# Performance work log

Hardware: AMD Instinct MI355X
Metric: run time of the kernel (lower is better)

## Reference

```python
import jax, jax.numpy as jnp
import numpy as np

COST_CLASS, COST_BBOX, COST_GIOU = 1.0, 5.0, 2.0


def _to_xyxy(b):
    cx, cy, w, h = b[..., 0], b[..., 1], b[..., 2], b[..., 3]
    return jnp.stack([cx - w / 2, cy - h / 2, cx + w / 2, cy + h / 2], axis=-1)


def _generalized_box_iou(a, b):
    # a: [N,4] xyxy, b: [M,4] xyxy -> [N,M]
    area_a = (a[:, 2] - a[:, 0]) * (a[:, 3] - a[:, 1])
    area_b = (b[:, 2] - b[:, 0]) * (b[:, 3] - b[:, 1])
    lt = jnp.maximum(a[:, None, :2], b[None, :, :2])
    rb = jnp.minimum(a[:, None, 2:], b[None, :, 2:])
    wh = jnp.clip(rb - lt, 0.0)
    inter = wh[..., 0] * wh[..., 1]
    union = area_a[:, None] + area_b[None, :] - inter
    iou = inter / union
    lt_c = jnp.minimum(a[:, None, :2], b[None, :, :2])
    rb_c = jnp.maximum(a[:, None, 2:], b[None, :, 2:])
    wh_c = jnp.clip(rb_c - lt_c, 0.0)
    area_c = wh_c[..., 0] * wh_c[..., 1]
    return iou - (area_c - union) / area_c


@jax.jit
def _cost_matrix(class_probs, pred_boxes, tgt_boxes, tgt_labels):
    bs, q, k = class_probs.shape
    probs_flat = class_probs.reshape(bs * q, k)
    cost_class = -probs_flat[:, tgt_labels]                          # [BQ, T]
    cost_bbox = jnp.abs(pred_boxes.reshape(bs * q, 1, 4) - tgt_boxes[None, :, :]).sum(-1)
    cost_giou = -_generalized_box_iou(_to_xyxy(pred_boxes.reshape(bs * q, 4)), _to_xyxy(tgt_boxes))
    C = COST_BBOX * cost_bbox + COST_CLASS * cost_class + COST_GIOU * cost_giou
    return C.reshape(bs, q, -1)


def _hungarian(cost):
    # min-cost assignment, cost [n, m] with n <= m (e-maxx JV algorithm).
    n, m = cost.shape
    INF = 1e18
    u = np.zeros(n + 1)
    v = np.zeros(m + 1)
    p = np.zeros(m + 1, dtype=np.int64)
    way = np.zeros(m + 1, dtype=np.int64)
    for i in range(1, n + 1):
        p[0] = i
        j0 = 0
        minv = np.full(m + 1, INF)
        used = np.zeros(m + 1, dtype=bool)
        while True:
            used[j0] = True
            i0 = p[j0]
            cj = cost[i0 - 1] - u[i0] - v[1:]
            upd = (~used[1:]) & (cj < minv[1:])
            minv[1:] = np.where(upd, cj, minv[1:])
            way[1:] = np.where(upd, j0, way[1:])
            free_vals = np.where(used[1:], INF, minv[1:])
            j1 = int(np.argmin(free_vals)) + 1
            delta = free_vals[j1 - 1]
            used_idx = np.nonzero(used)[0]
            u[p[used_idx]] += delta
            v[used_idx] -= delta
            minv[1:] = np.where(used[1:], minv[1:], minv[1:] - delta)
            j0 = j1
            if p[j0] == 0:
                break
        while j0:
            j1 = way[j0]
            p[j0] = p[j1]
            j0 = j1
    rows = p[1:] - 1                      # for each col: matched row or -1
    cols = np.nonzero(rows >= 0)[0]
    return rows[cols], cols               # (row_idx per match, col_idx) sorted by col


def setup_inputs() -> dict:
    key = jax.random.key(0)
    k1, k2, k3, k4 = jax.random.split(key, 4)
    bs, q, k, t_total = 64, 300, 91, 4096
    class_probs = jax.random.uniform(k1, (bs, q, k), dtype=jnp.float32)
    pred_boxes = jax.random.uniform(k2, (bs, q, 4), dtype=jnp.float32)
    tgt_boxes = jax.random.uniform(k3, (t_total, 4), dtype=jnp.float32)
    tgt_labels = jax.random.randint(k4, (t_total,), 0, k)
    return {"class_probs": class_probs, "pred_boxes": pred_boxes,
            "tgt_boxes": tgt_boxes, "tgt_labels": tgt_labels}


def reference(class_probs, pred_boxes, tgt_boxes, tgt_labels):
    bs, q, _ = class_probs.shape
    t_per = tgt_boxes.shape[0] // bs      # equal #targets per image
    C = _cost_matrix(class_probs, pred_boxes, tgt_boxes, tgt_labels)
    C_np = np.asarray(C)
    pred_idx, tgt_idx = [], []
    for b in range(bs):                   # per-batch assignment, as in the original
        c = C_np[b][:, b * t_per:(b + 1) * t_per]      # [Q, T], Q > T
        t_rows, q_cols = _hungarian(c.T)               # assign each target a query
        pred_idx.append(q_cols)
        tgt_idx.append(t_rows)
    return C, jnp.asarray(np.stack(pred_idx)), jnp.asarray(np.stack(tgt_idx))
```

## Files before the change

### kernel.cpp

```cpp
#include <hip/hip_runtime.h>

#define BS   64
#define Q    300
#define K    91
#define T    4096
#define TPER 64
#define M    300
#define NR   64
#define WS_STRIDE 304

typedef float __attribute__((ext_vector_type(4))) f32x4;

__device__ __forceinline__ float cost_entry(const float4 pb, const float4 tb,
                                            const float prob)
{
    const float px0 = pb.x - pb.z * 0.5f, py0 = pb.y - pb.w * 0.5f;
    const float px1 = pb.x + pb.z * 0.5f, py1 = pb.y + pb.w * 0.5f;
    const float parea = (px1 - px0) * (py1 - py0);
    const float tx0 = tb.x - tb.z * 0.5f, ty0 = tb.y - tb.w * 0.5f;
    const float tx1 = tb.x + tb.z * 0.5f, ty1 = tb.y + tb.w * 0.5f;
    const float tarea = (tx1 - tx0) * (ty1 - ty0);
    const float bb = fabsf(pb.x - tb.x) + fabsf(pb.y - tb.y)
                   + fabsf(pb.z - tb.z) + fabsf(pb.w - tb.w);
    const float iw = fmaxf(fminf(px1, tx1) - fmaxf(px0, tx0), 0.f);
    const float ih = fmaxf(fminf(py1, ty1) - fmaxf(py0, ty0), 0.f);
    const float inter = iw * ih;
    const float uni   = parea + tarea - inter;
    const float iou   = inter * __builtin_amdgcn_rcpf(uni);
    const float cw  = fmaxf(fmaxf(px1, tx1) - fminf(px0, tx0), 0.f);
    const float ch  = fmaxf(fmaxf(py1, ty1) - fminf(py0, ty0), 0.f);
    const float carea = cw * ch;
    const float giou  = iou - (carea - uni) * __builtin_amdgcn_rcpf(carea);
    return 5.0f * bb - prob - 2.0f * giou;
}

__device__ void cost_block(int cb, const float* __restrict__ probs,
                           const float* __restrict__ pboxes,
                           const float* __restrict__ tboxes,
                           const int* __restrict__ tlabels,
                           float* __restrict__ C)
{
    __shared__ __align__(16) float sprob4[K][4];
    const int tid = threadIdx.x;
    const int bq0 = cb * 4;
    for (int idx = tid; idx < 4 * K; idx += 64) {
        const int k = idx >> 2, r = idx & 3;
        sprob4[k][r] = probs[(size_t)(bq0 + r) * K + k];
    }
    float4 pbr[4];
#pragma unroll
    for (int r = 0; r < 4; ++r) pbr[r] = ((const float4*)pboxes)[bq0 + r];
    __syncthreads();

    const float4* tbv = (const float4*)tboxes;
    const int4*   lbv = (const int4*)tlabels;

    int4 lb = lbv[tid];
    float4 tb[4];
#pragma unroll
    for (int k = 0; k < 4; ++k) tb[k] = tbv[(tid << 2) + k];

#pragma unroll 1
    for (int c = 0; c < 16; ++c) {
        int4 lbn = {0, 0, 0, 0};
        float4 tbn[4];
        if (c < 15) {
            const int nt0 = ((c + 1) << 8) + (tid << 2);
            lbn = lbv[nt0 >> 2];
#pragma unroll
            for (int k = 0; k < 4; ++k) tbn[k] = tbv[nt0 + k];
        }
        const int labs[4] = { lb.x, lb.y, lb.z, lb.w };
        float4 pr[4];
#pragma unroll
        for (int k = 0; k < 4; ++k)
            pr[k] = *(const float4*)sprob4[labs[k]];

        const int t0 = (c << 8) + (tid << 2);
        float out[4][4];
#pragma unroll
        for (int k = 0; k < 4; ++k) {
#pragma unroll
            for (int r = 0; r < 4; ++r) {
                const float prk = (r == 0) ? pr[k].x : (r == 1) ? pr[k].y
                                : (r == 2) ? pr[k].z : pr[k].w;
                out[r][k] = cost_entry(pbr[r], tb[k], prk);
            }
        }
#pragma unroll
        for (int r = 0; r < 4; ++r) {
            f32x4 v = { out[r][0], out[r][1], out[r][2], out[r][3] };
            __builtin_nontemporal_store(
                v, (f32x4*)&C[(size_t)(bq0 + r) * T + t0]);
        }
        if (c < 15) {
            lb = lbn;
#pragma unroll
            for (int k = 0; k < 4; ++k) tb[k] = tbn[k];
        }
    }
}

__device__ void hungarian_block(int b, const float* __restrict__ probs,
                                const float* __restrict__ pboxes,
                                const float* __restrict__ tboxes,
                                const int* __restrict__ tlabels,
                                float* __restrict__ wslice,
                                float* __restrict__ pred_out,
                                float* __restrict__ tgt_out)
{
    __shared__ int p[M + 1];
    __shared__ int way[M + 1];
    __shared__ int rargArr[NR];
    const int tid = threadIdx.x;
    const bool lv = (tid < 60);
    const int c0 = lv ? 5 * tid : 0;

    float4 pbx[5];
#pragma unroll
    for (int s = 0; s < 5; ++s)
        pbx[s] = ((const float4*)pboxes)[b * Q + c0 + s];

    float rmin_f = 1e30f; int rarg = 0;
#pragma unroll 1
    for (int i = 0; i < NR; ++i) {
        const float4 tb = ((const float4*)tboxes)[b * TPER + i];
        const int lab = tlabels[b * TPER + i];
        const size_t pbase = (size_t)(b * Q + c0) * K + lab;
        float vals[5];
        float lmin = 1e30f; int lidx = 0x7fffffff;
#pragma unroll
        for (int s = 0; s < 5; ++s) {
            const float pr = probs[pbase + (size_t)s * K];
            vals[s] = cost_entry(pbx[s], tb, pr);
            if (lv && vals[s] < lmin) { lmin = vals[s]; lidx = c0 + s; }
        }
        if (lv) {
#pragma unroll
            for (int s = 0; s < 5; ++s)
                wslice[i * WS_STRIDE + c0 + s] = vals[s];
        }
        float rv = lv ? lmin : 1e30f; int ri = lidx;
#pragma unroll
        for (int off = 32; off > 0; off >>= 1) {
            const float ov = __shfl_xor(rv, off);
            const int   oi = __shfl_xor(ri, off);
            if (ov < rv || (ov == rv && oi < ri)) { rv = ov; ri = oi; }
        }
        if (tid == i) { rmin_f = rv; rarg = ri; }
    }
    double u_reg = (double)rmin_f;

    rargArr[tid] = rarg;
    for (int j = tid; j <= M; j += 64) p[j] = 0;
    __syncthreads();

    unsigned long long m0 = 0ull;
    if (tid == 0) {
#pragma unroll 1
        for (int r = 0; r < NR; ++r) {
            const int ac = rargArr[r] + 1;
            if (p[ac] == 0) { p[ac] = r + 1; m0 |= 1ull << r; }
        }
    }
    __syncthreads();
    const unsigned long long matchedRows = __shfl(m0, 0);

    double v_[5], minv_[5];
#pragma unroll
    for (int s = 0; s < 5; ++s) v_[s] = 0.0;
    const unsigned used0 = lv ? 0u : 0x1fu;

#pragma unroll 1
    for (int i = 1; i <= NR; ++i) {
        if ((matchedRows >> (i - 1)) & 1ull) continue;
        if (tid == 0) p[0] = i;
        unsigned usedmask = used0;
        bool inTree = false;
#pragma unroll
        for (int s = 0; s < 5; ++s) minv_[s] = 1e18;
        int i0 = i, j0 = 0;
        float crow[5];
        {
            const float* rp = wslice + (size_t)(i0 - 1) * WS_STRIDE + c0;
#pragma unroll
            for (int s = 0; s < 5; ++s) crow[s] = rp[s];
        }
        int guard = 0;
        while (true) {
            if (tid == i0 - 1) inTree = true;
            const double ui0 = __shfl(u_reg, i0 - 1);
            double lmin = 1e18; int lidx = 0x7fffffff;
#pragma unroll
            for (int s = 0; s < 5; ++s) {
                if (!((usedmask >> s) & 1u)) {
                    const double cj = (double)crow[s] - ui0 - v_[s];
                    if (cj < minv_[s]) { minv_[s] = cj; way[c0 + s + 1] = j0; }
                    if (minv_[s] < lmin) { lmin = minv_[s]; lidx = c0 + s; }
                }
            }
            double rv = lmin; int ri = lidx;
#pragma unroll
            for (int off = 32; off > 0; off >>= 1) {
                const double ov = __shfl_xor(rv, off);
                const int    oi = __shfl_xor(ri, off);
                if (ov < rv || (ov == rv && oi < ri)) { rv = ov; ri = oi; }
            }
            const double delta = rv;
            const int c1 = ri, j1 = c1 + 1;
            const int i0n = p[j1];
            float crow2[5];
            if (i0n) {
                const float* rp2 = wslice + (size_t)(i0n - 1) * WS_STRIDE + c0;
#pragma unroll
                for (int s = 0; s < 5; ++s) crow2[s] = rp2[s];
            }
            if (inTree) u_reg += delta;
#pragma unroll
            for (int s = 0; s < 5; ++s) {
                if ((usedmask >> s) & 1u) v_[s] -= delta;
                else                      minv_[s] -= delta;
            }
            if (lv && c1 >= c0 && c1 < c0 + 5) usedmask |= 1u << (c1 - c0);
            j0 = j1;
            if (!i0n || ++guard > 512) break;
            i0 = i0n;
#pragma unroll
            for (int s = 0; s < 5; ++s) crow[s] = crow2[s];
        }
        __syncthreads();
        if (tid == 0) {
            int jj = j0;
            while (jj) { const int jn = way[jj]; p[jj] = p[jn]; jj = jn; }
        }
        __syncthreads();
    }

    int cnt = 0;
#pragma unroll
    for (int s = 0; s < 5; ++s)
        if (lv && p[c0 + s + 1] > 0) ++cnt;
    int incl = cnt;
#pragma unroll
    for (int off = 1; off < 64; off <<= 1) {
        const int t = __shfl_up(incl, off);
        if (tid >= off) incl += t;
    }
    int pos = incl - cnt;
#pragma unroll
    for (int s = 0; s < 5; ++s) {
        if (lv) {
            const int pi = p[c0 + s + 1];
            if (pi > 0) {
                pred_out[b * TPER + pos] = (float)(c0 + s);
                tgt_out [b * TPER + pos] = (float)(pi - 1);
                ++pos;
            }
        }
    }
}

__global__ __launch_bounds__(64) void fused_kernel(
    const float* __restrict__ probs, const float* __restrict__ pboxes,
    const float* __restrict__ tboxes, const int* __restrict__ tlabels,
    float* __restrict__ C, float* __restrict__ pred_out,
    float* __restrict__ tgt_out, float* __restrict__ ws)
{
    const int bid = blockIdx.x;
    if (bid < BS)
        hungarian_block(bid, probs, pboxes, tboxes, tlabels,
                        ws + (size_t)bid * NR * WS_STRIDE, pred_out, tgt_out);
    else
        cost_block(bid - BS, probs, pboxes, tboxes, tlabels, C);
}

__global__ __launch_bounds__(256) void cost_kernel_fb(
    const float* __restrict__ probs, const float* __restrict__ pboxes,
    const float* __restrict__ tboxes, const int* __restrict__ tlabels,
    float* __restrict__ C)
{
    __shared__ float sprobs[4][K];
    const int tid = threadIdx.x;
    const int bq0 = blockIdx.x * 4;
    for (int idx = tid; idx < 4 * K; idx += 256)
        sprobs[idx / K][idx % K] = probs[(size_t)bq0 * K + idx];
    float4 pbr[4];
#pragma unroll
    for (int r = 0; r < 4; ++r) pbr[r] = ((const float4*)pboxes)[bq0 + r];
    __syncthreads();
#pragma unroll
    for (int c = 0; c < 4; ++c) {
        const int t0 = (c << 10) + (tid << 2);
        const int4 lb4 = *(const int4*)(tlabels + t0);
        float out[4][4];
#pragma unroll
        for (int k = 0; k < 4; ++k) {
            const float4 tb = ((const float4*)tboxes)[t0 + k];
            const int lab = (k == 0) ? lb4.x : (k == 1) ? lb4.y : (k == 2) ? lb4.z : lb4.w;
#pragma unroll
            for (int r = 0; r < 4; ++r)
                out[r][k] = cost_entry(pbr[r], tb, sprobs[r][lab]);
        }
#pragma unroll
        for (int r = 0; r < 4; ++r)
            *(float4*)&C[(size_t)(bq0 + r) * T + t0] =
                make_float4(out[r][0], out[r][1], out[r][2], out[r][3]);
    }
}

__global__ __launch_bounds__(64) void hungarian_kernel_fb(
    const float* __restrict__ C, float* __restrict__ pred_out,
    float* __restrict__ tgt_out)
{
    __shared__ float  cost[NR * M];
    __shared__ double v[M + 1], minv[M + 1], u[NR + 1];
    __shared__ int    p[M + 1], way[M + 1];
    __shared__ unsigned char used[M + 1];
    const int b = blockIdx.x;
    const int tid = threadIdx.x;
    const double INF = 1e18;
    for (int e = tid; e < NR * M; e += 64) {
        const int q = e >> 6, i = e & 63;
        cost[i * M + q] = C[(size_t)b * Q * T + (size_t)q * T + b * TPER + i];
    }
    for (int j = tid; j <= M; j += 64) { v[j] = 0.0; p[j] = 0; }
    for (int j = tid; j <= NR; j += 64) u[j] = 0.0;
    __syncthreads();
    for (int i = 1; i <= NR; ++i) {
        if (tid == 0) p[0] = i;
        for (int j = tid; j <= M; j += 64) { minv[j] = INF; used[j] = 0; }
        __syncthreads();
        int j0 = 0;
        while (true) {
            if (tid == 0) used[j0] = 1;
            __syncthreads();
            const int    i0  = p[j0];
            const double ui0 = u[i0];
            const float* crow = &cost[(i0 - 1) * M];
            double lmin = INF; int lidx = M + 1;
            for (int j = tid + 1; j <= M; j += 64) {
                if (!used[j]) {
                    double mv = minv[j];
                    const double cj = (double)crow[j - 1] - ui0 - v[j];
                    if (cj < mv) { mv = cj; minv[j] = cj; way[j] = j0; }
                    if (mv < lmin) { lmin = mv; lidx = j; }
                }
            }
#pragma unroll
            for (int off = 32; off > 0; off >>= 1) {
                const double oval = __shfl_down(lmin, off);
                const int    oidx = __shfl_down(lidx, off);
                if (oval < lmin || (oval == lmin && oidx < lidx)) { lmin = oval; lidx = oidx; }
            }
            const int    j1    = __shfl(lidx, 0);
            const double delta = __shfl(lmin, 0);
            __syncthreads();
            for (int j = tid; j <= M; j += 64) {
                if (used[j]) { u[p[j]] += delta; v[j] -= delta; }
                else          minv[j] -= delta;
            }
            __syncthreads();
            j0 = j1;
            if (p[j0] == 0) break;
        }
        if (tid == 0) {
            int jj = j0;
            while (jj) { const int j1 = way[jj]; p[jj] = p[j1]; jj = j1; }
        }
        __syncthreads();
    }
    if (tid == 0) {
        int kk = 0;
        for (int j = 1; j <= M; ++j) {
            if (p[j] > 0) {
                pred_out[b * TPER + kk] = (float)(j - 1);
                tgt_out [b * TPER + kk] = (float)(p[j] - 1);
                ++kk;
            }
        }
    }
}

extern "C" void kernel_launch(void* const* d_in, const int* in_sizes, int n_in,
                              void* d_out, int out_size, void* d_ws, size_t ws_size,
                              hipStream_t stream) {
    const float* probs   = (const float*)d_in[0];
    const float* pboxes  = (const float*)d_in[1];
    const float* tboxes  = (const float*)d_in[2];
    const int*   tlabels = (const int*)  d_in[3];

    float* C    = (float*)d_out;
    float* pred = C + (size_t)BS * Q * T;
    float* tgt  = pred + (size_t)BS * TPER;

    const size_t ws_needed = (size_t)BS * NR * WS_STRIDE * sizeof(float);
    if (ws_size >= ws_needed) {
        hipLaunchKernelGGL(fused_kernel, dim3(BS + BS * Q / 4), dim3(64), 0, stream,
                           probs, pboxes, tboxes, tlabels, C, pred, tgt, (float*)d_ws);
    } else {
        hipLaunchKernelGGL(cost_kernel_fb, dim3(BS * Q / 4), dim3(256), 0, stream,
                           probs, pboxes, tboxes, tlabels, C);
        hipLaunchKernelGGL(hungarian_kernel_fb, dim3(BS), dim3(64), 0, stream,
                           C, pred, tgt);
    }
}
```

Measured before the change: 410.9 us.

## Split fused launch into separate Hungarian and 256-thread cost kernels

Replaces the single fused launch, where the first 64 blocks ran the Hungarian solver and the rest computed the cost matrix, with two launches on the same stream: the Hungarian kernel first, then a standalone cost kernel. The cost kernel now uses 256-thread blocks that each cover 1024 targets per iteration, and the register-prefetch double buffering of target data is dropped. The aim is better occupancy and simpler scheduling of the cost computation. The trade-off is that the stream now serializes the two phases, so the long Hungarian chain no longer overlaps the cost writes.

New measurement: 471.4 us. 1.15x slower.

```diff
diff --git a/kernel.cpp b/kernel.cpp
--- a/kernel.cpp
+++ b/kernel.cpp
@@ -34,16 +34,17 @@
     return 5.0f * bb - prob - 2.0f * giou;
 }
 
-__device__ void cost_block(int cb, const float* __restrict__ probs,
-                           const float* __restrict__ pboxes,
-                           const float* __restrict__ tboxes,
-                           const int* __restrict__ tlabels,
-                           float* __restrict__ C)
+__global__ __launch_bounds__(256) void cost_kernel(
+    const float* __restrict__ probs,
+    const float* __restrict__ pboxes,
+    const float* __restrict__ tboxes,
+    const int*   __restrict__ tlabels,
+    float* __restrict__ C)
 {
     __shared__ __align__(16) float sprob4[K][4];
     const int tid = threadIdx.x;
-    const int bq0 = cb * 4;
-    for (int idx = tid; idx < 4 * K; idx += 64) {
+    const int bq0 = blockIdx.x * 4;
+    for (int idx = tid; idx < 4 * K; idx += 256) {
         const int k = idx >> 2, r = idx & 3;
         sprob4[k][r] = probs[(size_t)(bq0 + r) * K + k];
     }
@@ -55,63 +56,45 @@
     const float4* tbv = (const float4*)tboxes;
     const int4*   lbv = (const int4*)tlabels;
 
-    int4 lb = lbv[tid];
-    float4 tb[4];
-#pragma unroll
-    for (int k = 0; k < 4; ++k) tb[k] = tbv[(tid << 2) + k];
-
 #pragma unroll 1
-    for (int c = 0; c < 16; ++c) {
-        int4 lbn = {0, 0, 0, 0};
-        float4 tbn[4];
-        if (c < 15) {
-            const int nt0 = ((c + 1) << 8) + (tid << 2);
-            lbn = lbv[nt0 >> 2];
-#pragma unroll
-            for (int k = 0; k < 4; ++k) tbn[k] = tbv[nt0 + k];
-        }
+    for (int c = 0; c < 4; ++c) {
+        const int t0 = (c << 10) + (tid << 2);
+        const int4 lb = lbv[t0 >> 2];
         const int labs[4] = { lb.x, lb.y, lb.z, lb.w };
+        float4 tb[4];
         float4 pr[4];
 #pragma unroll
-        for (int k = 0; k < 4; ++k)
+        for (int k = 0; k < 4; ++k) {
+            tb[k] = tbv[t0 + k];
             pr[k] = *(const float4*)sprob4[labs[k]];
-
-        const int t0 = (c << 8) + (tid << 2);
-        float out[4][4];
-#pragma unroll
-        for (int k = 0; k < 4; ++k) {
-#pragma unroll
-            for (int r = 0; r < 4; ++r) {
+        }
+#pragma unroll
+        for (int r = 0; r < 4; ++r) {
+            float o[4];
+#pragma unroll
+            for (int k = 0; k < 4; ++k) {
                 const float prk = (r == 0) ? pr[k].x : (r == 1) ? pr[k].y
                                 : (r == 2) ? pr[k].z : pr[k].w;
-                out[r][k] = cost_entry(pbr[r], tb[k], prk);
-            }
-        }
-#pragma unroll
-        for (int r = 0; r < 4; ++r) {
-            f32x4 v = { out[r][0], out[r][1], out[r][2], out[r][3] };
+                o[k] = cost_entry(pbr[r], tb[k], prk);
+            }
+            f32x4 v = { o[0], o[1], o[2], o[3] };
             __builtin_nontemporal_store(
                 v, (f32x4*)&C[(size_t)(bq0 + r) * T + t0]);
         }
-        if (c < 15) {
-            lb = lbn;
-#pragma unroll
-            for (int k = 0; k < 4; ++k) tb[k] = tbn[k];
-        }
-    }
-}
-
-__device__ void hungarian_block(int b, const float* __restrict__ probs,
-                                const float* __restrict__ pboxes,
-                                const float* __restrict__ tboxes,
-                                const int* __restrict__ tlabels,
-                                float* __restrict__ wslice,
-                                float* __restrict__ pred_out,
-                                float* __restrict__ tgt_out)
+    }
+}
+
+__global__ __launch_bounds__(64) void hungarian_kernel(
+    const float* __restrict__ probs, const float* __restrict__ pboxes,
+    const float* __restrict__ tboxes, const int* __restrict__ tlabels,
+    float* __restrict__ ws, float* __restrict__ pred_out,
+    float* __restrict__ tgt_out)
 {
     __shared__ int p[M + 1];
     __shared__ int way[M + 1];
     __shared__ int rargArr[NR];
+    const int b = blockIdx.x;
+    float* __restrict__ wslice = ws + (size_t)b * NR * WS_STRIDE;
     const int tid = threadIdx.x;
     const bool lv = (tid < 60);
     const int c0 = lv ? 5 * tid : 0;
@@ -257,54 +240,6 @@
                 ++pos;
             }
         }
-    }
-}
-
-__global__ __launch_bounds__(64) void fused_kernel(
-    const float* __restrict__ probs, const float* __restrict__ pboxes,
-    const float* __restrict__ tboxes, const int* __restrict__ tlabels,
-    float* __restrict__ C, float* __restrict__ pred_out,
-    float* __restrict__ tgt_out, float* __restrict__ ws)
-{
-    const int bid = blockIdx.x;
-    if (bid < BS)
-        hungarian_block(bid, probs, pboxes, tboxes, tlabels,
-                        ws + (size_t)bid * NR * WS_STRIDE, pred_out, tgt_out);
-    else
-        cost_block(bid - BS, probs, pboxes, tboxes, tlabels, C);
-}
-
-__global__ __launch_bounds__(256) void cost_kernel_fb(
-    const float* __restrict__ probs, const float* __restrict__ pboxes,
-    const float* __restrict__ tboxes, const int* __restrict__ tlabels,
-    float* __restrict__ C)
-{
-    __shared__ float sprobs[4][K];
-    const int tid = threadIdx.x;
-    const int bq0 = blockIdx.x * 4;
-    for (int idx = tid; idx < 4 * K; idx += 256)
-        sprobs[idx / K][idx % K] = probs[(size_t)bq0 * K + idx];
-    float4 pbr[4];
-#pragma unroll
-    for (int r = 0; r < 4; ++r) pbr[r] = ((const float4*)pboxes)[bq0 + r];
-    __syncthreads();
-#pragma unroll
-    for (int c = 0; c < 4; ++c) {
-        const int t0 = (c << 10) + (tid << 2);
-        const int4 lb4 = *(const int4*)(tlabels + t0);
-        float out[4][4];
-#pragma unroll
-        for (int k = 0; k < 4; ++k) {
-            const float4 tb = ((const float4*)tboxes)[t0 + k];
-            const int lab = (k == 0) ? lb4.x : (k == 1) ? lb4.y : (k == 2) ? lb4.z : lb4.w;
-#pragma unroll
-            for (int r = 0; r < 4; ++r)
-                out[r][k] = cost_entry(pbr[r], tb, sprobs[r][lab]);
-        }
-#pragma unroll
-        for (int r = 0; r < 4; ++r)
-            *(float4*)&C[(size_t)(bq0 + r) * T + t0] =
-                make_float4(out[r][0], out[r][1], out[r][2], out[r][3]);
     }
 }
 
@@ -395,10 +330,12 @@
 
     const size_t ws_needed = (size_t)BS * NR * WS_STRIDE * sizeof(float);
     if (ws_size >= ws_needed) {
-        hipLaunchKernelGGL(fused_kernel, dim3(BS + BS * Q / 4), dim3(64), 0, stream,
-                           probs, pboxes, tboxes, tlabels, C, pred, tgt, (float*)d_ws);
+        hipLaunchKernelGGL(hungarian_kernel, dim3(BS), dim3(64), 0, stream,
+                           probs, pboxes, tboxes, tlabels, (float*)d_ws, pred, tgt);
+        hipLaunchKernelGGL(cost_kernel, dim3(BS * Q / 4), dim3(256), 0, stream,
+                           probs, pboxes, tboxes, tlabels, C);
     } else {
-        hipLaunchKernelGGL(cost_kernel_fb, dim3(BS * Q / 4), dim3(256), 0, stream,
+        hipLaunchKernelGGL(cost_kernel, dim3(BS * Q / 4), dim3(256), 0, stream,
                            probs, pboxes, tboxes, tlabels, C);
         hipLaunchKernelGGL(hungarian_kernel_fb, dim3(BS), dim3(64), 0, stream,
                            C, pred, tgt);
```
